# Optimization experiments

Measured on AMD Instinct MI355X. Metric: run time of the kernel, lower is better.

The kernel has to match this reference:

```python
import jax, jax.numpy as jnp
import numpy as np

NUM = 5  # grid intervals
K = 3    # spline order


def b_spline_basis(x, grid, k):
    """Cox-de Boor recursion. x: (B, D); grid: (D, G) with G = NUM+2k+1.
    Returns (B, D, NUM+k) basis values."""
    xe = x[:, :, None]                # (B, D, 1)
    g = grid[None, :, :]              # (1, D, G)
    # order-0: indicator of half-open interval [g_i, g_{i+1})
    B = ((xe >= g[:, :, :-1]) & (xe < g[:, :, 1:])).astype(x.dtype)
    for p in range(1, k + 1):
        B = ((xe - g[:, :, :-(p + 1)]) / (g[:, :, p:-1] - g[:, :, :-(p + 1)]) * B[:, :, :-1]
             + (g[:, :, p + 1:] - xe) / (g[:, :, p + 1:] - g[:, :, 1:-p]) * B[:, :, 1:])
    return B


def kan_layer(x, grid, coef, scale_base, scale_sp, mask):
    # x: (B, D)
    Bsp = b_spline_basis(x, grid, K)                                   # (B, D, NUM+K)
    out_sp = jnp.einsum('bdn,don,do->bo', Bsp, coef, scale_sp * mask)  # spline branch
    out_base = jnp.einsum('bd,do->bo', jax.nn.silu(x), scale_base * mask)  # residual silu branch
    return out_base + out_sp                                           # (B, out_dim)


def setup_inputs() -> dict:
    key = jax.random.key(0)
    k0, k1, k2, k3 = jax.random.split(key, 4)
    Bt, S, C, O = 2048, 128, 32, 3
    D = S * C  # in_dim = enc_in * seq_len = 4096
    x_enc = jax.random.uniform(k0, (Bt, S, C), jnp.float32, -1.0, 1.0)
    # extended grid over [-1, 1] with K extra knots each side (pykan extend_grid)
    h = 2.0 / NUM
    base = jnp.linspace(-1.0, 1.0, NUM + 1)
    grid1d = jnp.concatenate([base[0] - h * jnp.arange(K, 0, -1, dtype=jnp.float32),
                              base,
                              base[-1] + h * jnp.arange(1, K + 1, dtype=jnp.float32)])
    grid = jnp.tile(grid1d[None, :], (D, 1))                    # (D, NUM+2K+1)
    coef = 0.1 * jax.random.normal(k1, (D, O, NUM + K), jnp.float32)
    scale_base = (1.0 / np.sqrt(D)) * (1.0 + 0.1 * jax.random.normal(k2, (D, O), jnp.float32))
    scale_sp = jnp.full((D, O), 1.0 / np.sqrt(D), jnp.float32) + 0.0 * jax.random.normal(k3, (D, O))
    mask = jnp.ones((D, O), jnp.float32)
    return {
        'x_enc': x_enc,
        'x_mark_enc': jnp.zeros((1,), jnp.float32),
        'x_dec': jnp.zeros((1,), jnp.float32),
        'x_mark_dec': jnp.zeros((1,), jnp.float32),
        'grid': grid, 'coef': coef,
        'scale_base': scale_base, 'scale_sp': scale_sp, 'mask': mask,
    }


def reference(x_enc, x_mark_enc, x_dec, x_mark_dec, grid, coef, scale_base, scale_sp, mask):
    x = x_enc.reshape(x_enc.shape[0], -1)  # (B, enc_in*seq_len)
    return kan_layer(x, grid, coef, scale_base, scale_sp, mask)
```

## Files before the change

kernel.cpp:

```cpp
#include <hip/hip_runtime.h>
#include <math.h>

#define B_SZ   2048
#define D_SZ   4096
#define TB     16
#define NC     16
#define DC     256
#define NBG    (B_SZ / TB)

typedef float v2f __attribute__((ext_vector_type(2)));

#define WS_PART_BYTES  (NC * B_SZ * 3 * 4)

template<int CTRL>
__device__ __forceinline__ float dpp_add(float v) {
    int x = __builtin_amdgcn_update_dpp(0, __float_as_int(v), CTRL, 0xF, 0xF, true);
    return v + __int_as_float(x);
}
__device__ __forceinline__ float group16_sum(float v) {
    v = dpp_add<0x111>(v);
    v = dpp_add<0x112>(v);
    v = dpp_add<0x114>(v);
    v = dpp_add<0x118>(v);
    return v;
}
__device__ __forceinline__ v2f pk_fma(v2f a, v2f b, v2f c) {
    return __builtin_elementwise_fma(a, b, c);
}
__device__ __forceinline__ v2f splat(float s) { v2f v = {s, s}; return v; }

__global__ __launch_bounds__(256) void kan_fused(
    const float* __restrict__ x, const float* __restrict__ grid,
    const float* __restrict__ coef, const float* __restrict__ sb,
    const float* __restrict__ ssp,  const float* __restrict__ mask,
    float* __restrict__ partial)
{
    __shared__ float tl[TB * 16 * 3];

    const int tid = threadIdx.x;
    const int bg  = blockIdx.x;
    const int dc  = blockIdx.y;
    const int d   = dc * DC + tid;
    const int lane = tid & 63;

    const int b0 = bg * TB;
    const float* xp = x + (size_t)b0 * D_SZ + d;
    float xv[TB];
    #pragma unroll
    for (int q = 0; q < TB; ++q) xv[q] = xp[(size_t)q * D_SZ];

    float cps[27];
    #pragma unroll
    for (int o = 0; o < 3; ++o) {
        float m = mask[d*3 + o];
        float s = ssp[d*3 + o] * m;
        const float4* cvp = (const float4*)(coef + ((size_t)d*3 + o)*8);
        float4 ka = cvp[0], kb = cvp[1];
        float k[8] = {ka.x*s, ka.y*s, ka.z*s, ka.w*s,
                      kb.x*s, kb.y*s, kb.z*s, kb.w*s};
        float A3[5];
        #pragma unroll
        for (int c = 0; c < 5; ++c)
            A3[c] = (k[c+3] - k[c] + 3.0f*(k[c+1] - k[c+2])) * (1.0f/6.0f);
        cps[0*3+o] = (k[0] + 4.0f*k[1] + k[2]) * (1.0f/6.0f);
        cps[1*3+o] = (k[2] - k[0]) * 0.5f;
        cps[2*3+o] = (k[0] + k[2]) * 0.5f - k[1];
        cps[3*3+o] = A3[0];
        cps[4*3+o] = A3[1] - A3[0];
        cps[5*3+o] = A3[2] - A3[1];
        cps[6*3+o] = A3[3] - A3[2];
        cps[7*3+o] = A3[4] - A3[3];
        cps[8*3+o] = sb[d*3 + o] * m;
    }

    const float g3   = grid[3];
    const float invh = 1.0f / (grid[4] - grid[3]);
    const v2f invh2 = splat(invh);
    const v2f c0v   = splat(-g3 * invh);

    const v2f pc7 = splat(-17.0f/80640.0f);
    const v2f pc5 = splat(1.0f/480.0f);
    const v2f pc3 = splat(-1.0f/48.0f);
    const v2f pc1 = splat(0.25f);

    #pragma unroll
    for (int pr = 0; pr < TB/2; ++pr) {
        v2f X = {xv[2*pr], xv[2*pr + 1]};
        v2f u  = pk_fma(X, invh2, c0v);
        v2f u2 = u * u, u3 = u2 * u;
        v2f r1 = __builtin_elementwise_max(u - splat(1.0f), splat(0.0f));
        v2f r2 = __builtin_elementwise_max(u - splat(2.0f), splat(0.0f));
        v2f r3 = __builtin_elementwise_max(u - splat(3.0f), splat(0.0f));
        v2f r4 = __builtin_elementwise_max(u - splat(4.0f), splat(0.0f));
        v2f r13 = (r1*r1)*r1, r23 = (r2*r2)*r2, r33 = (r3*r3)*r3, r43 = (r4*r4)*r4;
        v2f y  = X * X;
        v2f pt = pk_fma(y, pc7, pc5);
        pt = pk_fma(y, pt, pc3);
        pt = pk_fma(y, pt, pc1);
        v2f sil = pk_fma(y, pt, X * splat(0.5f));

        #pragma unroll
        for (int o = 0; o < 3; ++o) {
            v2f a;
            a = pk_fma(u,   splat(cps[1*3+o]), splat(cps[0*3+o]));
            a = pk_fma(u2,  splat(cps[2*3+o]), a);
            a = pk_fma(u3,  splat(cps[3*3+o]), a);
            a = pk_fma(r13, splat(cps[4*3+o]), a);
            a = pk_fma(r23, splat(cps[5*3+o]), a);
            a = pk_fma(r33, splat(cps[6*3+o]), a);
            a = pk_fma(r43, splat(cps[7*3+o]), a);
            a = pk_fma(sil, splat(cps[8*3+o]), a);
            float s0 = group16_sum(a.x);
            float s1 = group16_sum(a.y);
            if ((lane & 15) == 15) {
                int g = tid >> 4;
                tl[((2*pr    )*16 + g)*3 + o] = s0;
                tl[((2*pr + 1)*16 + g)*3 + o] = s1;
            }
        }
    }

    __syncthreads();
    if (tid < TB*3) {
        int q = tid / 3, o = tid % 3;
        float s = 0.0f;
        #pragma unroll
        for (int g = 0; g < 16; ++g) s += tl[(q*16 + g)*3 + o];
        partial[((size_t)dc * B_SZ + (b0 + q))*3 + o] = s;
    }
}

__global__ __launch_bounds__(256) void reduce_partials(
    const float* __restrict__ partial, float* __restrict__ out)
{
    int i = blockIdx.x * 256 + threadIdx.x;
    if (i >= B_SZ * 3) return;
    float s = 0.0f;
    #pragma unroll
    for (int c = 0; c < NC; ++c) s += partial[(size_t)c * B_SZ * 3 + i];
    out[i] = s;
}

__global__ __launch_bounds__(256) void kan_fallback(
    const float* __restrict__ x, const float* __restrict__ grid,
    const float* __restrict__ coef, const float* __restrict__ sb,
    const float* __restrict__ ssp,  const float* __restrict__ mask,
    float* __restrict__ out)
{
    __shared__ float red[3][4];
    int b = blockIdx.x, tid = threadIdx.x;
    float g3 = grid[3], invh = 1.0f / (grid[4] - grid[3]);
    float acc[3] = {0.f, 0.f, 0.f};
    for (int i = 0; i < D_SZ / 256; ++i) {
        int d = i * 256 + tid;
        float xv = x[(size_t)b * D_SZ + d];
        float u  = (xv - g3) * invh;
        float cfl = floorf(u);
        cfl = fminf(fmaxf(cfl, 0.0f), 4.0f);
        int  cell = (int)cfl;
        float t  = u - cfl;
        float t2 = t * t, t3 = t2 * t;
        float omt = 1.0f - t;
        float w0 = omt*omt*omt * (1.0f/6.0f);
        float w1 = (3.0f*t3 - 6.0f*t2 + 4.0f) * (1.0f/6.0f);
        float w2 = (-3.0f*t3 + 3.0f*t2 + 3.0f*t + 1.0f) * (1.0f/6.0f);
        float w3 = t3 * (1.0f/6.0f);
        float sil = xv / (1.0f + __expf(-xv));
        #pragma unroll
        for (int o = 0; o < 3; ++o) {
            const float* cp = &coef[(d*3 + o) * 8 + cell];
            float s = w0*cp[0] + w1*cp[1] + w2*cp[2] + w3*cp[3];
            float m = mask[d*3 + o];
            acc[o] += s * ssp[d*3 + o] * m + sil * sb[d*3 + o] * m;
        }
    }
    int lane = tid & 63, wv = tid >> 6;
    #pragma unroll
    for (int o = 0; o < 3; ++o) {
        float v = acc[o];
        #pragma unroll
        for (int off = 32; off >= 1; off >>= 1) v += __shfl_down(v, off, 64);
        if (lane == 0) red[o][wv] = v;
    }
    __syncthreads();
    if (tid < 3) {
        float s = red[tid][0] + red[tid][1] + red[tid][2] + red[tid][3];
        out[b * 3 + tid] = s;
    }
}

extern "C" void kernel_launch(void* const* d_in, const int* in_sizes, int n_in,
                              void* d_out, int out_size, void* d_ws, size_t ws_size,
                              hipStream_t stream)
{
    const float* x    = (const float*)d_in[0];
    const float* grid = (const float*)d_in[4];
    const float* coef = (const float*)d_in[5];
    const float* sb   = (const float*)d_in[6];
    const float* ssp  = (const float*)d_in[7];
    const float* mask = (const float*)d_in[8];
    float* out = (float*)d_out;

    if (ws_size >= (size_t)WS_PART_BYTES) {
        float* partial = (float*)d_ws;
        dim3 g(NBG, NC);
        kan_fused<<<g, 256, 0, stream>>>(x, grid, coef, sb, ssp, mask, partial);
        reduce_partials<<<(B_SZ*3 + 255)/256, 256, 0, stream>>>(partial, out);
    } else {
        kan_fallback<<<B_SZ, 256, 0, stream>>>(x, grid, coef, sb, ssp, mask, out);
    }
}
```

Measured before the change: 22.32 us.

## Process two feature columns per thread and shorten cross-lane reduction

Each thread now handles two adjacent input features (float2 loads of x) and packs per-feature coefficients into v2f registers, so packed FMAs work on two features of the same batch row instead of two batch rows. The partial sums across the feature pair are added in-thread, which cuts the DPP reduction from 16 lanes to 4. Results go to a larger shared buffer summed with float4 reads. The D chunk count is halved to 8, so fewer partials need reducing. The cost is higher register pressure (27 v2f coefficients plus 16 float2 x values) and more shared-memory traffic per block.

After: 22.47 us. No clear change (+0.7%).

```diff
diff --git a/kernel.cpp b/kernel.cpp
--- a/kernel.cpp
+++ b/kernel.cpp
@@ -4,8 +4,8 @@
 #define B_SZ   2048
 #define D_SZ   4096
 #define TB     16
-#define NC     16
-#define DC     256
+#define NC     8
+#define DCB    512
 #define NBG    (B_SZ / TB)
 
 typedef float v2f __attribute__((ext_vector_type(2)));
@@ -17,11 +17,9 @@
     int x = __builtin_amdgcn_update_dpp(0, __float_as_int(v), CTRL, 0xF, 0xF, true);
     return v + __int_as_float(x);
 }
-__device__ __forceinline__ float group16_sum(float v) {
+__device__ __forceinline__ float group4_sum(float v) {
     v = dpp_add<0x111>(v);
     v = dpp_add<0x112>(v);
-    v = dpp_add<0x114>(v);
-    v = dpp_add<0x118>(v);
     return v;
 }
 __device__ __forceinline__ v2f pk_fma(v2f a, v2f b, v2f c) {
@@ -35,42 +33,47 @@
     const float* __restrict__ ssp,  const float* __restrict__ mask,
     float* __restrict__ partial)
 {
-    __shared__ float tl[TB * 16 * 3];
+    __shared__ float tl[TB * 3 * 64];
 
     const int tid = threadIdx.x;
     const int bg  = blockIdx.x;
     const int dc  = blockIdx.y;
-    const int d   = dc * DC + tid;
+    const int d0  = dc * DCB + 2 * tid;
     const int lane = tid & 63;
+    const int wv   = tid >> 6;
 
     const int b0 = bg * TB;
-    const float* xp = x + (size_t)b0 * D_SZ + d;
-    float xv[TB];
-    #pragma unroll
-    for (int q = 0; q < TB; ++q) xv[q] = xp[(size_t)q * D_SZ];
-
-    float cps[27];
-    #pragma unroll
-    for (int o = 0; o < 3; ++o) {
-        float m = mask[d*3 + o];
-        float s = ssp[d*3 + o] * m;
-        const float4* cvp = (const float4*)(coef + ((size_t)d*3 + o)*8);
-        float4 ka = cvp[0], kb = cvp[1];
-        float k[8] = {ka.x*s, ka.y*s, ka.z*s, ka.w*s,
-                      kb.x*s, kb.y*s, kb.z*s, kb.w*s};
-        float A3[5];
-        #pragma unroll
-        for (int c = 0; c < 5; ++c)
-            A3[c] = (k[c+3] - k[c] + 3.0f*(k[c+1] - k[c+2])) * (1.0f/6.0f);
-        cps[0*3+o] = (k[0] + 4.0f*k[1] + k[2]) * (1.0f/6.0f);
-        cps[1*3+o] = (k[2] - k[0]) * 0.5f;
-        cps[2*3+o] = (k[0] + k[2]) * 0.5f - k[1];
-        cps[3*3+o] = A3[0];
-        cps[4*3+o] = A3[1] - A3[0];
-        cps[5*3+o] = A3[2] - A3[1];
-        cps[6*3+o] = A3[3] - A3[2];
-        cps[7*3+o] = A3[4] - A3[3];
-        cps[8*3+o] = sb[d*3 + o] * m;
+    const float* xp = x + (size_t)b0 * D_SZ + d0;
+    float2 xv[TB];
+    #pragma unroll
+    for (int q = 0; q < TB; ++q) xv[q] = *(const float2*)(xp + (size_t)q * D_SZ);
+
+    v2f cpk[27];
+    #pragma unroll
+    for (int dd = 0; dd < 2; ++dd) {
+        const int d = d0 + dd;
+        #pragma unroll
+        for (int o = 0; o < 3; ++o) {
+            float m = mask[d*3 + o];
+            float s = ssp[d*3 + o] * m;
+            const float4* cvp = (const float4*)(coef + ((size_t)d*3 + o)*8);
+            float4 ka = cvp[0], kb = cvp[1];
+            float k[8] = {ka.x*s, ka.y*s, ka.z*s, ka.w*s,
+                          kb.x*s, kb.y*s, kb.z*s, kb.w*s};
+            float A3[5];
+            #pragma unroll
+            for (int c = 0; c < 5; ++c)
+                A3[c] = (k[c+3] - k[c] + 3.0f*(k[c+1] - k[c+2])) * (1.0f/6.0f);
+            cpk[0*3+o][dd] = (k[0] + 4.0f*k[1] + k[2]) * (1.0f/6.0f);
+            cpk[1*3+o][dd] = (k[2] - k[0]) * 0.5f;
+            cpk[2*3+o][dd] = (k[0] + k[2]) * 0.5f - k[1];
+            cpk[3*3+o][dd] = A3[0];
+            cpk[4*3+o][dd] = A3[1] - A3[0];
+            cpk[5*3+o][dd] = A3[2] - A3[1];
+            cpk[6*3+o][dd] = A3[3] - A3[2];
+            cpk[7*3+o][dd] = A3[4] - A3[3];
+            cpk[8*3+o][dd] = sb[d*3 + o] * m;
+        }
     }
 
     const float g3   = grid[3];
@@ -84,8 +87,8 @@
     const v2f pc1 = splat(0.25f);
 
     #pragma unroll
-    for (int pr = 0; pr < TB/2; ++pr) {
-        v2f X = {xv[2*pr], xv[2*pr + 1]};
+    for (int q = 0; q < TB; ++q) {
+        v2f X = {xv[q].x, xv[q].y};
         v2f u  = pk_fma(X, invh2, c0v);
         v2f u2 = u * u, u3 = u2 * u;
         v2f r1 = __builtin_elementwise_max(u - splat(1.0f), splat(0.0f));
@@ -102,30 +105,31 @@
         #pragma unroll
         for (int o = 0; o < 3; ++o) {
             v2f a;
-            a = pk_fma(u,   splat(cps[1*3+o]), splat(cps[0*3+o]));
-            a = pk_fma(u2,  splat(cps[2*3+o]), a);
-            a = pk_fma(u3,  splat(cps[3*3+o]), a);
-            a = pk_fma(r13, splat(cps[4*3+o]), a);
-            a = pk_fma(r23, splat(cps[5*3+o]), a);
-            a = pk_fma(r33, splat(cps[6*3+o]), a);
-            a = pk_fma(r43, splat(cps[7*3+o]), a);
-            a = pk_fma(sil, splat(cps[8*3+o]), a);
-            float s0 = group16_sum(a.x);
-            float s1 = group16_sum(a.y);
-            if ((lane & 15) == 15) {
-                int g = tid >> 4;
-                tl[((2*pr    )*16 + g)*3 + o] = s0;
-                tl[((2*pr + 1)*16 + g)*3 + o] = s1;
-            }
+            a = pk_fma(u,   cpk[1*3+o], cpk[0*3+o]);
+            a = pk_fma(u2,  cpk[2*3+o], a);
+            a = pk_fma(u3,  cpk[3*3+o], a);
+            a = pk_fma(r13, cpk[4*3+o], a);
+            a = pk_fma(r23, cpk[5*3+o], a);
+            a = pk_fma(r33, cpk[6*3+o], a);
+            a = pk_fma(r43, cpk[7*3+o], a);
+            a = pk_fma(sil, cpk[8*3+o], a);
+            float s = a.x + a.y;
+            s = group4_sum(s);
+            if ((lane & 3) == 3)
+                tl[(q*3 + o)*64 + wv*16 + (lane >> 2)] = s;
         }
     }
 
     __syncthreads();
     if (tid < TB*3) {
+        const float4* v = (const float4*)&tl[tid * 64];
+        float s = 0.0f;
+        #pragma unroll
+        for (int i = 0; i < 16; ++i) {
+            float4 t = v[i];
+            s += (t.x + t.y) + (t.z + t.w);
+        }
         int q = tid / 3, o = tid % 3;
-        float s = 0.0f;
-        #pragma unroll
-        for (int g = 0; g < 16; ++g) s += tl[(q*16 + g)*3 + o];
         partial[((size_t)dc * B_SZ + (b0 + q))*3 + o] = s;
     }
 }
```
